# Performance work log

Hardware: AMD Instinct MI355X
Metric: run time of the kernel (lower is better)

Reference implementation:

```python
import jax, jax.numpy as jnp
import numpy as np

P = 100_000      # distinct products
T = 300_000      # total product nodes after repeat_interleave (sum of cnt)
NQ = 100_000     # query nodes
B = 8192         # number of sessions (segments)
QIN = 128; PIN = 128; D = 128; MSL = 50; DL = D - MSL


def setup_inputs() -> dict:
    key = jax.random.key(0)
    ks = jax.random.split(key, 12)
    # irregular repeat counts in {1..5}, tiled so sum == 3*P == T exactly (static shape)
    cnt = jnp.asarray(np.tile(np.array([1, 2, 3, 4, 5], np.int32), P // 5))
    s = 0.05
    return {
        "query_feat": jax.random.normal(ks[0], (NQ, QIN), jnp.float32),
        "product_feat": jax.random.normal(ks[1], (P, PIN), jnp.float32),
        "Wq": jax.random.normal(ks[2], (DL, QIN), jnp.float32) * s,
        "bq": jnp.zeros((DL,), jnp.float32),
        "Wp": jax.random.normal(ks[3], (DL, PIN), jnp.float32) * s,
        "bp": jnp.zeros((DL,), jnp.float32),
        "pos_table": jax.random.normal(ks[4], (MSL, MSL), jnp.float32) * s,
        "Wn": jax.random.normal(ks[5], (D, D), jnp.float32) * s,
        "bn": jnp.zeros((D,), jnp.float32),
        "Wc": jax.random.normal(ks[6], (D, D), jnp.float32) * s,
        "Wa": jax.random.normal(ks[7], (1, D), jnp.float32) * s,
        "query_pos_id": jax.random.randint(ks[8], (NQ,), 0, MSL, jnp.int32),
        "product_pos_id": jax.random.randint(ks[9], (T,), 0, MSL, jnp.int32),
        "query_batch": jax.random.randint(ks[10], (NQ,), 0, B, jnp.int32),
        "product_batch": jax.random.randint(ks[11], (P,), 0, B, jnp.int32),
        "cnt": cnt,
        "num_segments": B,
        "total_product_nodes": T,
    }


def _segment_mean(x, seg, num_segments):
    sums = jax.ops.segment_sum(x, seg, num_segments=num_segments)
    counts = jax.ops.segment_sum(jnp.ones((x.shape[0],), x.dtype), seg, num_segments=num_segments)
    return sums / jnp.maximum(counts, 1.0)[:, None]


def reference(query_feat, product_feat, Wq, bq, Wp, bp, pos_table, Wn, bn, Wc, Wa,
              query_pos_id, product_pos_id, query_batch, product_batch, cnt,
              num_segments, total_product_nodes):
    # query branch: linear -> concat positional embedding -> tanh  [NQ, D]
    qe = jnp.tanh(jnp.concatenate([query_feat @ Wq.T + bq, pos_table[query_pos_id]], axis=1))
    # product branch: linear, repeat_interleave by cnt, concat pos emb, tanh  [T, D]
    pe = product_feat @ Wp.T + bp
    pe = jnp.repeat(pe, cnt, axis=0, total_repeat_length=total_product_nodes)
    pe = jnp.tanh(jnp.concatenate([pe, pos_table[product_pos_id]], axis=1))
    pbatch = jnp.repeat(product_batch, cnt, axis=0, total_repeat_length=total_product_nodes)
    # stack nodes (products first, then queries — matches torch.concat order)
    node_emb = jnp.concatenate([pe, qe], axis=0)            # [N, D]
    node_batch = jnp.concatenate([pbatch, query_batch], axis=0)
    # coarse session representation: segment mean, broadcast back to nodes
    coarse = _segment_mean(node_emb, node_batch, num_segments)  # [B, D]
    coarse_g = coarse[node_batch]                                # [N, D]
    # attention gating
    att = jax.nn.sigmoid(node_emb @ Wn.T + bn + coarse_g @ Wc.T) @ Wa.T  # [N, 1]
    weighted = node_emb * att
    return _segment_mean(weighted, node_batch, num_segments)    # [B, D]
```

## Files before the change

### kernel.cpp

```cpp
#include <hip/hip_runtime.h>
#include <hip/hip_bf16.h>
#include <math.h>


constexpr int D   = 128;
constexpr int DL  = 78;
constexpr int MSL = 50;
constexpr int RP  = 80;

typedef __attribute__((ext_vector_type(8))) short bfrag8;
typedef __attribute__((ext_vector_type(4))) float facc4;
typedef __attribute__((ext_vector_type(4))) short short4v;

__device__ __forceinline__ float sigmoidf_(float x) {
    return 1.f / (1.f + __expf(-x));
}

__device__ __forceinline__ float waveSum(float v) {
    #pragma unroll
    for (int m = 1; m < 64; m <<= 1) v += __shfl_xor(v, m, 64);
    return v;
}

__device__ __forceinline__ char* ldsAddr(__hip_bfloat16* base, int row, int byte_in_row) {
    return reinterpret_cast<char*>(base) + row * 256 + (byte_in_row ^ ((row & 7) << 4));
}
__device__ __forceinline__ bfrag8 ldsR16(const __hip_bfloat16* base, int row, int byte_in_row) {
    return *reinterpret_cast<const bfrag8*>(
        reinterpret_cast<const char*>(base) + row * 256 + (byte_in_row ^ ((row & 7) << 4)));
}
__device__ __forceinline__ short4v ldsR8(const __hip_bfloat16* base, int row, int byte_in_row) {
    return *reinterpret_cast<const short4v*>(
        reinterpret_cast<const char*>(base) + row * 256 + (byte_in_row ^ ((row & 7) << 4)));
}

__global__ __launch_bounds__(256) void k_tables2(
    const float* __restrict__ pos_table, const float* __restrict__ Wn,
    float* __restrict__ tpos, float* __restrict__ posWn) {
    __shared__ float tposL[MSL * MSL];
    int t = threadIdx.x;
    for (int o = t; o < MSL * MSL; o += 256) tposL[o] = tanhf(pos_table[o]);
    __syncthreads();
    if (blockIdx.x == 0)
        for (int o = t; o < MSL * MSL; o += 256) tpos[o] = tposL[o];
    for (int o = blockIdx.x * 256 + t; o < MSL * D; o += gridDim.x * 256) {
        int r = o >> 7, d = o & 127;
        float acc = 0.f;
        #pragma unroll 10
        for (int j = 0; j < MSL; ++j) acc += tposL[r * MSL + j] * Wn[d * D + DL + j];
        posWn[o] = acc;
    }
}

__global__ __launch_bounds__(256) void k_convW(
    const float* __restrict__ Wq, const float* __restrict__ Wp, const float* __restrict__ Wn,
    __hip_bfloat16* __restrict__ Wqbf, __hip_bfloat16* __restrict__ Wpbf,
    __hip_bfloat16* __restrict__ Wnbf) {
    int i = blockIdx.x * 256 + threadIdx.x;
    if (i < 80 * 128) {
        int n = i >> 7;
        Wqbf[i] = __float2bfloat16((n < DL) ? Wq[i] : 0.f);
        Wpbf[i] = __float2bfloat16((n < DL) ? Wp[i] : 0.f);
    } else if (i < 80 * 128 + 128 * 128) {
        int o = i - 80 * 128;
        int j = o & 127;
        Wnbf[o] = __float2bfloat16((j < DL) ? Wn[o] : 0.f);
    }
}

__global__ void k_scanA(const int* __restrict__ cnt, int P, int* __restrict__ chunkSum) {
    __shared__ int s[256];
    int p = blockIdx.x * 256 + threadIdx.x;
    s[threadIdx.x] = (p < P) ? cnt[p] : 0;
    __syncthreads();
    for (int st = 128; st > 0; st >>= 1) {
        if (threadIdx.x < st) s[threadIdx.x] += s[threadIdx.x + st];
        __syncthreads();
    }
    if (threadIdx.x == 0) chunkSum[blockIdx.x] = s[0];
}
__global__ __launch_bounds__(1024) void k_scanB(
    const int* __restrict__ chunkSum, int nC, int* __restrict__ chunkOff) {
    __shared__ int s[1024];
    int t = threadIdx.x;
    int carry = 0;
    for (int base = 0; base < nC; base += 1024) {
        int v = (base + t < nC) ? chunkSum[base + t] : 0;
        s[t] = v;
        __syncthreads();
        for (int st = 1; st < 1024; st <<= 1) {
            int add = (t >= st) ? s[t - st] : 0;
            __syncthreads();
            s[t] += add;
            __syncthreads();
        }
        if (base + t < nC) chunkOff[base + t] = carry + s[t] - v;
        carry += s[1023];
        __syncthreads();
    }
}
__global__ void k_scanC(const int* __restrict__ cnt, int P, const int* __restrict__ chunkOff,
                        int* __restrict__ prodOff) {
    __shared__ int s[256];
    int t = threadIdx.x;
    int p = blockIdx.x * 256 + t;
    int v = (p < P) ? cnt[p] : 0;
    s[t] = v;
    __syncthreads();
    for (int st = 1; st < 256; st <<= 1) {
        int add = (t >= st) ? s[t - st] : 0;
        __syncthreads();
        s[t] += add;
        __syncthreads();
    }
    if (p < P) prodOff[p] = chunkOff[blockIdx.x] + s[t] - v;
}

template <bool IS_QUERY>
__global__ __launch_bounds__(256) void k_branch(
    const float* __restrict__ feat, const __hip_bfloat16* __restrict__ Wbf,
    const float* __restrict__ bias, const __hip_bfloat16* __restrict__ Wnbf,
    const int* __restrict__ batch, const int* __restrict__ posid,
    const int* __restrict__ cnt, int Nrows,
    __hip_bfloat16* __restrict__ tE, __hip_bfloat16* __restrict__ eWn,
    float* __restrict__ segsum, float* __restrict__ segcnt, int* __restrict__ hist) {
    __shared__ __hip_bfloat16 featL[64 * 128];
    __shared__ __hip_bfloat16 linL[64 * 128];
    int t = threadIdx.x;
    int r0 = blockIdx.x * 64;

    {
        int r = t >> 2, c = t & 3;
        int gr = r0 + r;
        #pragma unroll
        for (int j = 0; j < 8; ++j) {
            int kf = c * 32 + j * 4;
            float4 v = make_float4(0.f, 0.f, 0.f, 0.f);
            if (gr < Nrows) v = *reinterpret_cast<const float4*>(&feat[(size_t)gr * 128 + kf]);
            __hip_bfloat16 tmp[4] = {__float2bfloat16(v.x), __float2bfloat16(v.y),
                                     __float2bfloat16(v.z), __float2bfloat16(v.w)};
            *reinterpret_cast<short4v*>(ldsAddr(featL, r, kf * 2)) = *reinterpret_cast<short4v*>(tmp);
        }
        if (c < 2) {
            short4v z = {0, 0, 0, 0};
            *reinterpret_cast<short4v*>(ldsAddr(linL, r, 160 + c * 16)) = z;
            *reinterpret_cast<short4v*>(ldsAddr(linL, r, 168 + c * 16)) = z;
        }
    }
    __syncthreads();

    int l = t & 63, w = t >> 6;
    int lr = l & 15, lq = l >> 4;
    int am = w * 16 + lr;

    bfrag8 a[4];
    #pragma unroll
    for (int kt = 0; kt < 4; ++kt) a[kt] = ldsR16(featL, am, kt * 64 + lq * 16);
    facc4 c1[5];
    #pragma unroll
    for (int nt = 0; nt < 5; ++nt) { facc4 z = {0.f, 0.f, 0.f, 0.f}; c1[nt] = z; }
    #pragma unroll
    for (int nt = 0; nt < 5; ++nt) {
        #pragma unroll
        for (int kt = 0; kt < 4; ++kt) {
            bfrag8 b = *reinterpret_cast<const bfrag8*>(&Wbf[(nt * 16 + lr) * 128 + kt * 32 + lq * 8]);
            c1[nt] = __builtin_amdgcn_mfma_f32_16x16x32_bf16(a[kt], b, c1[nt], 0, 0, 0);
        }
    }

    int   bj[4];
    float mult[4];
    bool  valid[4];
    #pragma unroll
    for (int j = 0; j < 4; ++j) {
        int m = w * 16 + lq * 4 + j;
        int gr = r0 + m;
        valid[j] = gr < Nrows;
        bj[j]    = valid[j] ? batch[gr] : 0;
        mult[j]  = IS_QUERY ? 1.f : (valid[j] ? (float)cnt[gr] : 0.f);
    }
    #pragma unroll
    for (int nt = 0; nt < 5; ++nt) {
        int n = nt * 16 + lr;
        float bs = (n < DL) ? bias[n] : 0.f;
        #pragma unroll
        for (int j = 0; j < 4; ++j) {
            int m = w * 16 + lq * 4 + j;
            float tv = (n < DL) ? tanhf(c1[nt][j] + bs) : 0.f;
            *reinterpret_cast<__hip_bfloat16*>(ldsAddr(linL, m, 2 * n)) = __float2bfloat16(tv);
            if (n < DL && valid[j])
                atomicAdd(&segsum[(size_t)bj[j] * D + n], mult[j] * tv);
        }
    }
    __syncthreads();

    {
        int r = t >> 2, c = t & 3;
        int gr = r0 + r;
        #pragma unroll
        for (int j = 0; j < 5; ++j) {
            int byte = c * 40 + j * 8;
            short4v v = ldsR8(linL, r, byte);
            if (gr < Nrows)
                *reinterpret_cast<short4v*>(&tE[(size_t)gr * RP + c * 20 + j * 4]) = v;
        }
    }

    bfrag8 a2[3];
    #pragma unroll
    for (int kt = 0; kt < 3; ++kt) a2[kt] = ldsR16(linL, am, kt * 64 + lq * 16);
    facc4 c2[8];
    #pragma unroll
    for (int nt = 0; nt < 8; ++nt) { facc4 z = {0.f, 0.f, 0.f, 0.f}; c2[nt] = z; }
    #pragma unroll
    for (int nt = 0; nt < 8; ++nt) {
        #pragma unroll
        for (int kt = 0; kt < 3; ++kt) {
            bfrag8 b = *reinterpret_cast<const bfrag8*>(&Wnbf[(nt * 16 + lr) * 128 + kt * 32 + lq * 8]);
            c2[nt] = __builtin_amdgcn_mfma_f32_16x16x32_bf16(a2[kt], b, c2[nt], 0, 0, 0);
        }
    }
    #pragma unroll
    for (int nt = 0; nt < 8; ++nt) {
        int d2 = nt * 16 + lr;
        #pragma unroll
        for (int j = 0; j < 4; ++j) {
            int m = w * 16 + lq * 4 + j;
            *reinterpret_cast<__hip_bfloat16*>(ldsAddr(featL, m, 2 * d2)) =
                __float2bfloat16(c2[nt][j]);
        }
    }
    __syncthreads();

    {
        int r = t >> 2, c = t & 3;
        int gr = r0 + r;
        #pragma unroll
        for (int j = 0; j < 4; ++j) {
            int byte = c * 64 + j * 16;
            bfrag8 v = ldsR16(featL, r, byte);
            if (gr < Nrows)
                *reinterpret_cast<bfrag8*>(&eWn[(size_t)gr * 128 + c * 32 + j * 8]) = v;
        }
    }

    if (t < 64) {
        int gr = r0 + t;
        if (gr < Nrows) {
            int b = batch[gr];
            if (IS_QUERY) {
                atomicAdd(&segcnt[b], 1.f);
                atomicAdd(&hist[b * MSL + posid[gr]], 1);
            } else {
                atomicAdd(&segcnt[b], (float)cnt[gr]);
            }
        }
    }
}

__global__ void k_hist_prod(const int* __restrict__ ppos, const int* __restrict__ pbatch,
                            const int* __restrict__ prodOff, const int* __restrict__ cnt,
                            int P, int* __restrict__ hist) {
    int p = blockIdx.x * 256 + threadIdx.x;
    if (p >= P) return;
    int b = pbatch[p], off = prodOff[p], c = cnt[p];
    for (int j = 0; j < c; ++j) atomicAdd(&hist[b * MSL + ppos[off + j]], 1);
}

__global__ void k_possum(const int* __restrict__ hist, const float* __restrict__ tpos,
                         int B, float* __restrict__ segsum) {
    int t = threadIdx.x;
    int bb = t / MSL, k = t - bb * MSL;
    if (bb >= 5) return;
    int b = blockIdx.x * 5 + bb;
    if (b >= B) return;
    float acc = 0.f;
    for (int r = 0; r < MSL; ++r) acc += (float)hist[b * MSL + r] * tpos[r * MSL + k];
    segsum[(size_t)b * D + DL + k] = acc;
}

__global__ __launch_bounds__(256) void k_coarse(
    const float* __restrict__ segsum, const float* __restrict__ segcnt,
    const float* __restrict__ Wc, const float* __restrict__ bn, int B,
    float* __restrict__ coarseWc) {
    __shared__ __hip_bfloat16 WcL[128 * 130];
    __shared__ float cL[16 * 128];
    int t = threadIdx.x;
    int b0 = blockIdx.x * 16;
    for (int o = t; o < D * D; o += 256) {
        int d = o >> 7, k = o & 127;
        WcL[d * 130 + k] = __float2bfloat16(Wc[o]);
    }
    for (int o = t; o < 16 * D; o += 256) {
        int bb = o >> 7, d = o & 127;
        int b = b0 + bb;
        cL[o] = (b < B) ? segsum[(size_t)b * D + d] / fmaxf(segcnt[b], 1.f) : 0.f;
    }
    __syncthreads();
    for (int o = t; o < 16 * D; o += 256) {
        int bb = o >> 7, d = o & 127;
        int b = b0 + bb;
        if (b >= B) continue;
        float acc = bn[d];
        const float* cr = &cL[bb * 128];
        const __hip_bfloat16* wr = &WcL[d * 130];
        #pragma unroll 8
        for (int j = 0; j < D; ++j) acc += cr[j] * __bfloat162float(wr[j]);
        coarseWc[(size_t)b * D + d] = acc;
    }
}

__global__ __launch_bounds__(256) void k_att_prod(
    const __hip_bfloat16* __restrict__ pWn, const __hip_bfloat16* __restrict__ tp,
    const float* __restrict__ coarseWc, const float* __restrict__ posWn,
    const float* __restrict__ tpos, const float* __restrict__ Wa,
    const int* __restrict__ pbatch, const int* __restrict__ prodOff,
    const int* __restrict__ cnt, const int* __restrict__ ppos,
    int P, float* __restrict__ out) {
    int p = blockIdx.x * 4 + (threadIdx.x >> 6);
    int l = threadIdx.x & 63;
    if (p >= P) return;
    int b = pbatch[p], off = prodOff[p], c = cnt[p];
    float base0 = __bfloat162float(pWn[(size_t)p * D + l])      + coarseWc[(size_t)b * D + l];
    float base1 = __bfloat162float(pWn[(size_t)p * D + 64 + l]) + coarseWc[(size_t)b * D + 64 + l];
    float wa0 = Wa[l], wa1 = Wa[64 + l];
    float attsum = 0.f, posacc = 0.f;
    for (int j = 0; j < c; ++j) {
        int pos = ppos[off + j];
        float z0 = base0 + posWn[pos * D + l];
        float z1 = base1 + posWn[pos * D + 64 + l];
        float part = sigmoidf_(z0) * wa0 + sigmoidf_(z1) * wa1;
        float att = waveSum(part);
        attsum += att;
        if (l >= 14) posacc += att * tpos[pos * MSL + (l - 14)];
    }
    float t0 = __bfloat162float(tp[(size_t)p * RP + l]);
    atomicAdd(&out[(size_t)b * D + l], attsum * t0);
    if (l < 14) {
        float t1 = __bfloat162float(tp[(size_t)p * RP + 64 + l]);
        atomicAdd(&out[(size_t)b * D + 64 + l], attsum * t1);
    } else {
        atomicAdd(&out[(size_t)b * D + 64 + l], posacc);
    }
}

__global__ __launch_bounds__(256) void k_att_query(
    const __hip_bfloat16* __restrict__ qWn, const __hip_bfloat16* __restrict__ tq,
    const float* __restrict__ coarseWc, const float* __restrict__ posWn,
    const float* __restrict__ tpos, const float* __restrict__ Wa,
    const int* __restrict__ qbatch, const int* __restrict__ qpos,
    int NQ, float* __restrict__ out) {
    int q = blockIdx.x * 4 + (threadIdx.x >> 6);
    int l = threadIdx.x & 63;
    if (q >= NQ) return;
    int b = qbatch[q], pos = qpos[q];
    float z0 = __bfloat162float(qWn[(size_t)q * D + l])      + coarseWc[(size_t)b * D + l]      + posWn[pos * D + l];
    float z1 = __bfloat162float(qWn[(size_t)q * D + 64 + l]) + coarseWc[(size_t)b * D + 64 + l] + posWn[pos * D + 64 + l];
    float part = sigmoidf_(z0) * Wa[l] + sigmoidf_(z1) * Wa[64 + l];
    float att = waveSum(part);
    float e0 = __bfloat162float(tq[(size_t)q * RP + l]);
    atomicAdd(&out[(size_t)b * D + l], att * e0);
    float e1 = (l < 14) ? __bfloat162float(tq[(size_t)q * RP + 64 + l]) : tpos[pos * MSL + (l - 14)];
    atomicAdd(&out[(size_t)b * D + 64 + l], att * e1);
}

__global__ void k_final(float* __restrict__ out, const float* __restrict__ segcnt, int B) {
    int i = blockIdx.x * 256 + threadIdx.x;
    if (i < B * D) out[i] = out[i] / fmaxf(segcnt[i >> 7], 1.f);
}

extern "C" void kernel_launch(void* const* d_in, const int* in_sizes, int n_in,
                              void* d_out, int out_size, void* d_ws, size_t ws_size,
                              hipStream_t stream) {
    const float* query_feat   = (const float*)d_in[0];
    const float* product_feat = (const float*)d_in[1];
    const float* Wq = (const float*)d_in[2];
    const float* bq = (const float*)d_in[3];
    const float* Wp = (const float*)d_in[4];
    const float* bp = (const float*)d_in[5];
    const float* pos_table = (const float*)d_in[6];
    const float* Wn = (const float*)d_in[7];
    const float* bn = (const float*)d_in[8];
    const float* Wc = (const float*)d_in[9];
    const float* Wa = (const float*)d_in[10];
    const int* qpos   = (const int*)d_in[11];
    const int* ppos   = (const int*)d_in[12];
    const int* qbatch = (const int*)d_in[13];
    const int* pbatch = (const int*)d_in[14];
    const int* cnt    = (const int*)d_in[15];

    int NQ = in_sizes[11];
    int P  = in_sizes[15];
    int B  = out_size / D;
    float* out = (float*)d_out;

    char* w = (char*)d_ws;
    size_t off = 0;
    auto take = [&](size_t bytes) -> char* {
        char* p = w + off;
        off = (off + bytes + 255) & ~(size_t)255;
        return p;
    };
    float* segsum = (float*)take((size_t)B * D * 4);
    float* segcnt = (float*)take((size_t)B * 4);
    int*   hist   = (int*)  take((size_t)B * MSL * 4);
    size_t zeroBytes = off;
    float* coarseWc = (float*)take((size_t)B * D * 4);
    float* tpos  = (float*)take(MSL * MSL * 4);
    float* posWn = (float*)take(MSL * D * 4);
    __hip_bfloat16* Wqbf = (__hip_bfloat16*)take(80 * 128 * 2);
    __hip_bfloat16* Wpbf = (__hip_bfloat16*)take(80 * 128 * 2);
    __hip_bfloat16* Wnbf = (__hip_bfloat16*)take(128 * 128 * 2);
    int nC = (P + 255) / 256;
    int* chunkSum = (int*)take((size_t)nC * 4);
    int* chunkOff = (int*)take((size_t)nC * 4);
    int* prodOff  = (int*)take((size_t)P * 4);
    __hip_bfloat16* tq  = (__hip_bfloat16*)take((size_t)NQ * RP * 2);
    __hip_bfloat16* tp  = (__hip_bfloat16*)take((size_t)P * RP * 2);
    __hip_bfloat16* qWn = (__hip_bfloat16*)take((size_t)NQ * D * 2);
    __hip_bfloat16* pWn = (__hip_bfloat16*)take((size_t)P * D * 2);
    (void)ws_size; (void)n_in;

    hipMemsetAsync(segsum, 0, zeroBytes, stream);
    hipMemsetAsync(out, 0, (size_t)out_size * 4, stream);

    hipLaunchKernelGGL(k_tables2, dim3(8), dim3(256), 0, stream, pos_table, Wn, tpos, posWn);
    hipLaunchKernelGGL(k_convW, dim3((80 * 128 + 128 * 128 + 255) / 256), dim3(256), 0, stream,
                       Wq, Wp, Wn, Wqbf, Wpbf, Wnbf);
    hipLaunchKernelGGL(k_scanA, dim3(nC), dim3(256), 0, stream, cnt, P, chunkSum);
    hipLaunchKernelGGL(k_scanB, dim3(1), dim3(1024), 0, stream, chunkSum, nC, chunkOff);
    hipLaunchKernelGGL(k_scanC, dim3(nC), dim3(256), 0, stream, cnt, P, chunkOff, prodOff);

    hipLaunchKernelGGL((k_branch<true>), dim3((NQ + 63) / 64), dim3(256), 0, stream,
                       query_feat, Wqbf, bq, Wnbf, qbatch, qpos, (const int*)nullptr, NQ,
                       tq, qWn, segsum, segcnt, hist);
    hipLaunchKernelGGL((k_branch<false>), dim3((P + 63) / 64), dim3(256), 0, stream,
                       product_feat, Wpbf, bp, Wnbf, pbatch, (const int*)nullptr, cnt, P,
                       tp, pWn, segsum, segcnt, hist);
    hipLaunchKernelGGL(k_hist_prod, dim3((P + 255) / 256), dim3(256), 0, stream,
                       ppos, pbatch, prodOff, cnt, P, hist);
    hipLaunchKernelGGL(k_possum, dim3((B + 4) / 5), dim3(256), 0, stream, hist, tpos, B, segsum);
    hipLaunchKernelGGL(k_coarse, dim3((B + 15) / 16), dim3(256), 0, stream,
                       segsum, segcnt, Wc, bn, B, coarseWc);

    hipLaunchKernelGGL(k_att_prod, dim3((P + 3) / 4), dim3(256), 0, stream,
                       pWn, tp, coarseWc, posWn, tpos, Wa, pbatch, prodOff, cnt, ppos, P, out);
    hipLaunchKernelGGL(k_att_query, dim3((NQ + 3) / 4), dim3(256), 0, stream,
                       qWn, tq, coarseWc, posWn, tpos, Wa, qbatch, qpos, NQ, out);
    hipLaunchKernelGGL(k_final, dim3((B * D + 255) / 256), dim3(256), 0, stream, out, segcnt, B);
}
```

Measured before the change: 380.4 us.

## Merge query/product branch and attention kernels, load features directly into MFMA registers

Combines the query and product branch kernels into one launch that picks its path per block, and folds the product position histogram into it. Feature rows are now read from global memory straight into MFMA A fragments, which removes the LDS staging buffer and one barrier. The eWn output is written directly as scattered bf16 stores instead of going through LDS, trading coalescing for fewer syncs. The two attention kernels are merged into one launch, and the per-repeat wave reductions are unrolled into five independent reduction chains to expose ILP, at the cost of always evaluating five slots.

Result: faster. 311.1 us (-18.2%).

```diff
diff --git a/kernel.cpp b/kernel.cpp
--- a/kernel.cpp
+++ b/kernel.cpp
@@ -16,12 +16,6 @@
     return 1.f / (1.f + __expf(-x));
 }
 
-__device__ __forceinline__ float waveSum(float v) {
-    #pragma unroll
-    for (int m = 1; m < 64; m <<= 1) v += __shfl_xor(v, m, 64);
-    return v;
-}
-
 __device__ __forceinline__ char* ldsAddr(__hip_bfloat16* base, int row, int byte_in_row) {
     return reinterpret_cast<char*>(base) + row * 256 + (byte_in_row ^ ((row & 7) << 4));
 }
@@ -32,6 +26,14 @@
 __device__ __forceinline__ short4v ldsR8(const __hip_bfloat16* base, int row, int byte_in_row) {
     return *reinterpret_cast<const short4v*>(
         reinterpret_cast<const char*>(base) + row * 256 + (byte_in_row ^ ((row & 7) << 4)));
+}
+
+__device__ __forceinline__ bfrag8 cvt8(float4 a, float4 b) {
+    __hip_bfloat16 t[8] = {__float2bfloat16(a.x), __float2bfloat16(a.y),
+                           __float2bfloat16(a.z), __float2bfloat16(a.w),
+                           __float2bfloat16(b.x), __float2bfloat16(b.y),
+                           __float2bfloat16(b.z), __float2bfloat16(b.w)};
+    return *reinterpret_cast<bfrag8*>(t);
 }
 
 __global__ __launch_bounds__(256) void k_tables2(
@@ -116,46 +118,50 @@
     if (p < P) prodOff[p] = chunkOff[blockIdx.x] + s[t] - v;
 }
 
-template <bool IS_QUERY>
-__global__ __launch_bounds__(256) void k_branch(
-    const float* __restrict__ feat, const __hip_bfloat16* __restrict__ Wbf,
-    const float* __restrict__ bias, const __hip_bfloat16* __restrict__ Wnbf,
-    const int* __restrict__ batch, const int* __restrict__ posid,
-    const int* __restrict__ cnt, int Nrows,
-    __hip_bfloat16* __restrict__ tE, __hip_bfloat16* __restrict__ eWn,
+__global__ __launch_bounds__(256, 3) void k_branch2(
+    const float* __restrict__ qfeat, const float* __restrict__ pfeat,
+    const __hip_bfloat16* __restrict__ Wqbf, const __hip_bfloat16* __restrict__ Wpbf,
+    const float* __restrict__ bq, const float* __restrict__ bp,
+    const __hip_bfloat16* __restrict__ Wnbf,
+    const int* __restrict__ qbatch, const int* __restrict__ pbatch,
+    const int* __restrict__ qpos, const int* __restrict__ ppos,
+    const int* __restrict__ cnt, const int* __restrict__ prodOff,
+    int NQ, int P, int qBlocks,
+    __hip_bfloat16* __restrict__ tq, __hip_bfloat16* __restrict__ tp,
+    __hip_bfloat16* __restrict__ qWn, __hip_bfloat16* __restrict__ pWn,
     float* __restrict__ segsum, float* __restrict__ segcnt, int* __restrict__ hist) {
-    __shared__ __hip_bfloat16 featL[64 * 128];
+    const bool isQ = (int)blockIdx.x < qBlocks;
+    const int r0 = (isQ ? blockIdx.x : blockIdx.x - qBlocks) * 64;
+    const float* feat = isQ ? qfeat : pfeat;
+    const __hip_bfloat16* Wbf = isQ ? Wqbf : Wpbf;
+    const float* bias = isQ ? bq : bp;
+    const int* batch = isQ ? qbatch : pbatch;
+    const int Nrows = isQ ? NQ : P;
+    __hip_bfloat16* tE  = isQ ? tq : tp;
+    __hip_bfloat16* eWn = isQ ? qWn : pWn;
+
     __shared__ __hip_bfloat16 linL[64 * 128];
     int t = threadIdx.x;
-    int r0 = blockIdx.x * 64;
-
-    {
-        int r = t >> 2, c = t & 3;
-        int gr = r0 + r;
-        #pragma unroll
-        for (int j = 0; j < 8; ++j) {
-            int kf = c * 32 + j * 4;
-            float4 v = make_float4(0.f, 0.f, 0.f, 0.f);
-            if (gr < Nrows) v = *reinterpret_cast<const float4*>(&feat[(size_t)gr * 128 + kf]);
-            __hip_bfloat16 tmp[4] = {__float2bfloat16(v.x), __float2bfloat16(v.y),
-                                     __float2bfloat16(v.z), __float2bfloat16(v.w)};
-            *reinterpret_cast<short4v*>(ldsAddr(featL, r, kf * 2)) = *reinterpret_cast<short4v*>(tmp);
-        }
-        if (c < 2) {
-            short4v z = {0, 0, 0, 0};
-            *reinterpret_cast<short4v*>(ldsAddr(linL, r, 160 + c * 16)) = z;
-            *reinterpret_cast<short4v*>(ldsAddr(linL, r, 168 + c * 16)) = z;
-        }
-    }
-    __syncthreads();
-
     int l = t & 63, w = t >> 6;
     int lr = l & 15, lq = l >> 4;
     int am = w * 16 + lr;
 
+    if (t < 64) {
+        bfrag8 z = {0, 0, 0, 0, 0, 0, 0, 0};
+        *reinterpret_cast<bfrag8*>(ldsAddr(linL, t, 160)) = z;
+        *reinterpret_cast<bfrag8*>(ldsAddr(linL, t, 176)) = z;
+    }
+
+    int gra = r0 + am;
+    const float* frow = &feat[(size_t)(gra < Nrows ? gra : Nrows - 1) * 128];
     bfrag8 a[4];
     #pragma unroll
-    for (int kt = 0; kt < 4; ++kt) a[kt] = ldsR16(featL, am, kt * 64 + lq * 16);
+    for (int kt = 0; kt < 4; ++kt) {
+        float4 u = *reinterpret_cast<const float4*>(&frow[kt * 32 + lq * 8]);
+        float4 v = *reinterpret_cast<const float4*>(&frow[kt * 32 + lq * 8 + 4]);
+        a[kt] = cvt8(u, v);
+    }
+
     facc4 c1[5];
     #pragma unroll
     for (int nt = 0; nt < 5; ++nt) { facc4 z = {0.f, 0.f, 0.f, 0.f}; c1[nt] = z; }
@@ -177,7 +183,7 @@
         int gr = r0 + m;
         valid[j] = gr < Nrows;
         bj[j]    = valid[j] ? batch[gr] : 0;
-        mult[j]  = IS_QUERY ? 1.f : (valid[j] ? (float)cnt[gr] : 0.f);
+        mult[j]  = isQ ? 1.f : (valid[j] ? (float)cnt[gr] : 0.f);
     }
     #pragma unroll
     for (int nt = 0; nt < 5; ++nt) {
@@ -199,8 +205,7 @@
         int gr = r0 + r;
         #pragma unroll
         for (int j = 0; j < 5; ++j) {
-            int byte = c * 40 + j * 8;
-            short4v v = ldsR8(linL, r, byte);
+            short4v v = ldsR8(linL, r, c * 40 + j * 8);
             if (gr < Nrows)
                 *reinterpret_cast<short4v*>(&tE[(size_t)gr * RP + c * 20 + j * 4]) = v;
         }
@@ -221,26 +226,13 @@
         }
     }
     #pragma unroll
-    for (int nt = 0; nt < 8; ++nt) {
-        int d2 = nt * 16 + lr;
-        #pragma unroll
-        for (int j = 0; j < 4; ++j) {
-            int m = w * 16 + lq * 4 + j;
-            *reinterpret_cast<__hip_bfloat16*>(ldsAddr(featL, m, 2 * d2)) =
-                __float2bfloat16(c2[nt][j]);
-        }
-    }
-    __syncthreads();
-
-    {
-        int r = t >> 2, c = t & 3;
-        int gr = r0 + r;
-        #pragma unroll
-        for (int j = 0; j < 4; ++j) {
-            int byte = c * 64 + j * 16;
-            bfrag8 v = ldsR16(featL, r, byte);
-            if (gr < Nrows)
-                *reinterpret_cast<bfrag8*>(&eWn[(size_t)gr * 128 + c * 32 + j * 8]) = v;
+    for (int j = 0; j < 4; ++j) {
+        int m = w * 16 + lq * 4 + j;
+        int gr = r0 + m;
+        if (gr < Nrows) {
+            #pragma unroll
+            for (int nt = 0; nt < 8; ++nt)
+                eWn[(size_t)gr * 128 + nt * 16 + lr] = __float2bfloat16(c2[nt][j]);
         }
     }
 
@@ -248,23 +240,17 @@
         int gr = r0 + t;
         if (gr < Nrows) {
             int b = batch[gr];
-            if (IS_QUERY) {
+            if (isQ) {
                 atomicAdd(&segcnt[b], 1.f);
-                atomicAdd(&hist[b * MSL + posid[gr]], 1);
+                atomicAdd(&hist[b * MSL + qpos[gr]], 1);
             } else {
-                atomicAdd(&segcnt[b], (float)cnt[gr]);
+                int c = cnt[gr], off2 = prodOff[gr];
+                atomicAdd(&segcnt[b], (float)c);
+                for (int j = 0; j < c; ++j)
+                    atomicAdd(&hist[b * MSL + ppos[off2 + j]], 1);
             }
         }
     }
-}
-
-__global__ void k_hist_prod(const int* __restrict__ ppos, const int* __restrict__ pbatch,
-                            const int* __restrict__ prodOff, const int* __restrict__ cnt,
-                            int P, int* __restrict__ hist) {
-    int p = blockIdx.x * 256 + threadIdx.x;
-    if (p >= P) return;
-    int b = pbatch[p], off = prodOff[p], c = cnt[p];
-    for (int j = 0; j < c; ++j) atomicAdd(&hist[b * MSL + ppos[off + j]], 1);
 }
 
 __global__ void k_possum(const int* __restrict__ hist, const float* __restrict__ tpos,
@@ -310,58 +296,68 @@
     }
 }
 
-__global__ __launch_bounds__(256) void k_att_prod(
+__global__ __launch_bounds__(256) void k_att(
     const __hip_bfloat16* __restrict__ pWn, const __hip_bfloat16* __restrict__ tp,
-    const float* __restrict__ coarseWc, const float* __restrict__ posWn,
-    const float* __restrict__ tpos, const float* __restrict__ Wa,
-    const int* __restrict__ pbatch, const int* __restrict__ prodOff,
-    const int* __restrict__ cnt, const int* __restrict__ ppos,
-    int P, float* __restrict__ out) {
-    int p = blockIdx.x * 4 + (threadIdx.x >> 6);
-    int l = threadIdx.x & 63;
-    if (p >= P) return;
-    int b = pbatch[p], off = prodOff[p], c = cnt[p];
-    float base0 = __bfloat162float(pWn[(size_t)p * D + l])      + coarseWc[(size_t)b * D + l];
-    float base1 = __bfloat162float(pWn[(size_t)p * D + 64 + l]) + coarseWc[(size_t)b * D + 64 + l];
-    float wa0 = Wa[l], wa1 = Wa[64 + l];
-    float attsum = 0.f, posacc = 0.f;
-    for (int j = 0; j < c; ++j) {
-        int pos = ppos[off + j];
-        float z0 = base0 + posWn[pos * D + l];
-        float z1 = base1 + posWn[pos * D + 64 + l];
-        float part = sigmoidf_(z0) * wa0 + sigmoidf_(z1) * wa1;
-        float att = waveSum(part);
-        attsum += att;
-        if (l >= 14) posacc += att * tpos[pos * MSL + (l - 14)];
-    }
-    float t0 = __bfloat162float(tp[(size_t)p * RP + l]);
-    atomicAdd(&out[(size_t)b * D + l], attsum * t0);
-    if (l < 14) {
-        float t1 = __bfloat162float(tp[(size_t)p * RP + 64 + l]);
-        atomicAdd(&out[(size_t)b * D + 64 + l], attsum * t1);
-    } else {
-        atomicAdd(&out[(size_t)b * D + 64 + l], posacc);
-    }
-}
-
-__global__ __launch_bounds__(256) void k_att_query(
     const __hip_bfloat16* __restrict__ qWn, const __hip_bfloat16* __restrict__ tq,
     const float* __restrict__ coarseWc, const float* __restrict__ posWn,
     const float* __restrict__ tpos, const float* __restrict__ Wa,
-    const int* __restrict__ qbatch, const int* __restrict__ qpos,
-    int NQ, float* __restrict__ out) {
-    int q = blockIdx.x * 4 + (threadIdx.x >> 6);
-    int l = threadIdx.x & 63;
-    if (q >= NQ) return;
-    int b = qbatch[q], pos = qpos[q];
-    float z0 = __bfloat162float(qWn[(size_t)q * D + l])      + coarseWc[(size_t)b * D + l]      + posWn[pos * D + l];
-    float z1 = __bfloat162float(qWn[(size_t)q * D + 64 + l]) + coarseWc[(size_t)b * D + 64 + l] + posWn[pos * D + 64 + l];
-    float part = sigmoidf_(z0) * Wa[l] + sigmoidf_(z1) * Wa[64 + l];
-    float att = waveSum(part);
-    float e0 = __bfloat162float(tq[(size_t)q * RP + l]);
-    atomicAdd(&out[(size_t)b * D + l], att * e0);
-    float e1 = (l < 14) ? __bfloat162float(tq[(size_t)q * RP + 64 + l]) : tpos[pos * MSL + (l - 14)];
-    atomicAdd(&out[(size_t)b * D + 64 + l], att * e1);
+    const int* __restrict__ pbatch, const int* __restrict__ qbatch,
+    const int* __restrict__ prodOff, const int* __restrict__ cnt,
+    const int* __restrict__ ppos, const int* __restrict__ qpos,
+    int P, int NQ, int pBlocks, float* __restrict__ out) {
+    int wv = threadIdx.x >> 6, l = threadIdx.x & 63;
+    if ((int)blockIdx.x < pBlocks) {
+        int p = blockIdx.x * 4 + wv;
+        if (p >= P) return;
+        int b = pbatch[p], off = prodOff[p], c = cnt[p];
+        float base0 = __bfloat162float(pWn[(size_t)p * D + l])      + coarseWc[(size_t)b * D + l];
+        float base1 = __bfloat162float(pWn[(size_t)p * D + 64 + l]) + coarseWc[(size_t)b * D + 64 + l];
+        float wa0 = Wa[l], wa1 = Wa[64 + l];
+        float part[5];
+        int   posr[5];
+        #pragma unroll
+        for (int j = 0; j < 5; ++j) {
+            bool on = j < c;
+            int pos = on ? ppos[off + j] : 0;
+            posr[j] = pos;
+            float z0 = base0 + posWn[pos * D + l];
+            float z1 = base1 + posWn[pos * D + 64 + l];
+            part[j] = on ? (sigmoidf_(z0) * wa0 + sigmoidf_(z1) * wa1) : 0.f;
+        }
+        #pragma unroll
+        for (int m = 1; m < 64; m <<= 1) {
+            #pragma unroll
+            for (int j = 0; j < 5; ++j) part[j] += __shfl_xor(part[j], m, 64);
+        }
+        float attsum = part[0] + part[1] + part[2] + part[3] + part[4];
+        float posacc = 0.f;
+        if (l >= 14) {
+            #pragma unroll
+            for (int j = 0; j < 5; ++j)
+                posacc += part[j] * tpos[posr[j] * MSL + (l - 14)];
+        }
+        float t0 = __bfloat162float(tp[(size_t)p * RP + l]);
+        atomicAdd(&out[(size_t)b * D + l], attsum * t0);
+        if (l < 14) {
+            float t1 = __bfloat162float(tp[(size_t)p * RP + 64 + l]);
+            atomicAdd(&out[(size_t)b * D + 64 + l], attsum * t1);
+        } else {
+            atomicAdd(&out[(size_t)b * D + 64 + l], posacc);
+        }
+    } else {
+        int q = (blockIdx.x - pBlocks) * 4 + wv;
+        if (q >= NQ) return;
+        int b = qbatch[q], pos = qpos[q];
+        float z0 = __bfloat162float(qWn[(size_t)q * D + l])      + coarseWc[(size_t)b * D + l]      + posWn[pos * D + l];
+        float z1 = __bfloat162float(qWn[(size_t)q * D + 64 + l]) + coarseWc[(size_t)b * D + 64 + l] + posWn[pos * D + 64 + l];
+        float part = sigmoidf_(z0) * Wa[l] + sigmoidf_(z1) * Wa[64 + l];
+        #pragma unroll
+        for (int m = 1; m < 64; m <<= 1) part += __shfl_xor(part, m, 64);
+        float e0 = __bfloat162float(tq[(size_t)q * RP + l]);
+        atomicAdd(&out[(size_t)b * D + l], part * e0);
+        float e1 = (l < 14) ? __bfloat162float(tq[(size_t)q * RP + 64 + l]) : tpos[pos * MSL + (l - 14)];
+        atomicAdd(&out[(size_t)b * D + 64 + l], part * e1);
+    }
 }
 
 __global__ void k_final(float* __restrict__ out, const float* __restrict__ segcnt, int B) {
@@ -431,21 +427,19 @@
     hipLaunchKernelGGL(k_scanB, dim3(1), dim3(1024), 0, stream, chunkSum, nC, chunkOff);
     hipLaunchKernelGGL(k_scanC, dim3(nC), dim3(256), 0, stream, cnt, P, chunkOff, prodOff);
 
-    hipLaunchKernelGGL((k_branch<true>), dim3((NQ + 63) / 64), dim3(256), 0, stream,
-                       query_feat, Wqbf, bq, Wnbf, qbatch, qpos, (const int*)nullptr, NQ,
-                       tq, qWn, segsum, segcnt, hist);
-    hipLaunchKernelGGL((k_branch<false>), dim3((P + 63) / 64), dim3(256), 0, stream,
-                       product_feat, Wpbf, bp, Wnbf, pbatch, (const int*)nullptr, cnt, P,
-                       tp, pWn, segsum, segcnt, hist);
-    hipLaunchKernelGGL(k_hist_prod, dim3((P + 255) / 256), dim3(256), 0, stream,
-                       ppos, pbatch, prodOff, cnt, P, hist);
+    int qBlocks = (NQ + 63) / 64, pBlocksBr = (P + 63) / 64;
+    hipLaunchKernelGGL(k_branch2, dim3(qBlocks + pBlocksBr), dim3(256), 0, stream,
+                       query_feat, product_feat, Wqbf, Wpbf, bq, bp, Wnbf,
+                       qbatch, pbatch, qpos, ppos, cnt, prodOff, NQ, P, qBlocks,
+                       tq, tp, qWn, pWn, segsum, segcnt, hist);
+
     hipLaunchKernelGGL(k_possum, dim3((B + 4) / 5), dim3(256), 0, stream, hist, tpos, B, segsum);
     hipLaunchKernelGGL(k_coarse, dim3((B + 15) / 16), dim3(256), 0, stream,
                        segsum, segcnt, Wc, bn, B, coarseWc);
 
-    hipLaunchKernelGGL(k_att_prod, dim3((P + 3) / 4), dim3(256), 0, stream,
-                       pWn, tp, coarseWc, posWn, tpos, Wa, pbatch, prodOff, cnt, ppos, P, out);
-    hipLaunchKernelGGL(k_att_query, dim3((NQ + 3) / 4), dim3(256), 0, stream,
-                       qWn, tq, coarseWc, posWn, tpos, Wa, qbatch, qpos, NQ, out);
+    int pBlocksAtt = (P + 3) / 4, qBlocksAtt = (NQ + 3) / 4;
+    hipLaunchKernelGGL(k_att, dim3(pBlocksAtt + qBlocksAtt), dim3(256), 0, stream,
+                       pWn, tp, qWn, tq, coarseWc, posWn, tpos, Wa,
+                       pbatch, qbatch, prodOff, cnt, ppos, qpos, P, NQ, pBlocksAtt, out);
     hipLaunchKernelGGL(k_final, dim3((B * D + 255) / 256), dim3(256), 0, stream, out, segcnt, B);
 }
```
